# Kernel tuning notes

Hardware: AMD Instinct MI355X
Metric: run time of the kernel (lower is better)

The kernel has to match this reference:

```python
import jax, jax.numpy as jnp
import numpy as np

E = 16        # n_routed_experts
K = 2         # n_activated_experts (top-k)
DIM = 1024    # model dim
INTER = 704   # moe_inter_dim
B, S = 4, 1024


def setup_inputs() -> dict:
    key = jax.random.key(0)
    ks = jax.random.split(key, 5)
    x = jax.random.normal(ks[0], (B, S, DIM), dtype=jnp.float32)
    Wg = jax.random.normal(ks[1], (E, DIM), dtype=jnp.float32) * 0.02   # gate (Linear, no bias)
    W1 = jax.random.normal(ks[2], (E, DIM, INTER), dtype=jnp.float32) * 0.02
    W3 = jax.random.normal(ks[3], (E, DIM, INTER), dtype=jnp.float32) * 0.02
    W2 = jax.random.normal(ks[4], (E, INTER, DIM), dtype=jnp.float32) * 0.02
    return {"x": x, "Wg": Wg, "W1": W1, "W2": W2, "W3": W3}


def reference(x, Wg, W1, W2, W3):
    # Single-process semantics of MoEWithAll2All: the all2all dispatch/combine is
    # pure communication; the math is: softmax router -> top-k -> renormalize ->
    # per-expert SwiGLU MLP on routed tokens -> weighted combine at original slots.
    Bb, Ss, D = x.shape
    xf = x.reshape(-1, D)                              # [N, D], N = B*S
    logits = xf @ Wg.T                                 # [N, E]
    probs = jax.nn.softmax(logits, axis=-1)
    topw, topi = jax.lax.top_k(probs, K)               # [N, K]
    topw = topw / topw.sum(axis=-1, keepdims=True)
    # gates[n, e] = routed weight of token n for expert e (0 if not routed):
    # identical math to the masked gather/scatter dispatch in the original.
    gates = (jax.nn.one_hot(topi, E, dtype=xf.dtype) * topw[..., None]).sum(axis=1)  # [N, E]
    out = jnp.zeros_like(xf)
    for e in range(E):                                 # small fixed loop over experts
        h = jax.nn.silu(xf @ W1[e]) * (xf @ W3[e])     # SwiGLU expert, [N, INTER]
        out = out + gates[:, e:e + 1] * (h @ W2[e])    # combine with gate weights
    return out.reshape(Bb, Ss, D)
```

## Files before the change

kernel.cpp:

```cpp
#include <hip/hip_runtime.h>

#define NTOK 4096
#define DDIM 1024
#define IDIM 704
#define NEXP 16
#define NSLOT 8192
#define MAXT 128
#define NPAD1 768

typedef __attribute__((ext_vector_type(8))) short bf16x8;
typedef __attribute__((ext_vector_type(4))) float f32x4;
typedef __attribute__((ext_vector_type(4))) unsigned short us4;
typedef __attribute__((ext_vector_type(8))) unsigned short us8;

__device__ __forceinline__ unsigned short f2bf(float f) {
  union { float f; unsigned int u; } v; v.f = f;
  unsigned int r = v.u + 0x7fffu + ((v.u >> 16) & 1u);
  return (unsigned short)(r >> 16);
}

__device__ __forceinline__ void gload_lds16(const void* g, void* l) {
  __builtin_amdgcn_global_load_lds((const __attribute__((address_space(1))) void*)g,
                                   (__attribute__((address_space(3))) void*)l, 16, 0, 0);
}

__global__ void k_router(const float* __restrict__ x, const float* __restrict__ Wg,
                         int* __restrict__ tok_e, float* __restrict__ tok_w,
                         unsigned short* __restrict__ Xb) {
  int lane = threadIdx.x & 63;
  int wv = threadIdx.x >> 6;
  int t = blockIdx.x * 4 + wv;
  const f32x4* xr = (const f32x4*)(x + (size_t)t * DDIM);
  us4* xbr = (us4*)(Xb + (size_t)t * DDIM);
  f32x4 xv[4];
#pragma unroll
  for (int c = 0; c < 4; ++c) {
    xv[c] = xr[c * 64 + lane];
    us4 o;
#pragma unroll
    for (int j = 0; j < 4; ++j) o[j] = f2bf(xv[c][j]);
    xbr[c * 64 + lane] = o;
  }
  float p[NEXP];
#pragma unroll
  for (int e = 0; e < NEXP; ++e) {
    const f32x4* wr = (const f32x4*)(Wg + (size_t)e * DDIM);
    float s = 0.f;
#pragma unroll
    for (int c = 0; c < 4; ++c) {
      f32x4 w4 = wr[c * 64 + lane];
      s += xv[c][0]*w4[0] + xv[c][1]*w4[1] + xv[c][2]*w4[2] + xv[c][3]*w4[3];
    }
    p[e] = s;
  }
#pragma unroll
  for (int off = 32; off >= 1; off >>= 1) {
#pragma unroll
    for (int e = 0; e < NEXP; ++e) p[e] += __shfl_xor(p[e], off);
  }
  int i0 = 0; float b0 = p[0];
#pragma unroll
  for (int e = 1; e < NEXP; ++e) if (p[e] > b0) { b0 = p[e]; i0 = e; }
  int i1 = -1; float b1 = -3.4e38f;
#pragma unroll
  for (int e = 0; e < NEXP; ++e) if (e != i0 && p[e] > b1) { b1 = p[e]; i1 = e; }
  if (lane == 0) {
    float w0 = 1.f / (1.f + __expf(b1 - b0));
    tok_e[2*t] = i0; tok_e[2*t+1] = i1;
    tok_w[2*t] = w0; tok_w[2*t+1] = 1.f - w0;
  }
}

__global__ void k_scan_scatter(const int* __restrict__ tok_e, const float* __restrict__ tok_w,
                               int* __restrict__ counts, int* __restrict__ offsets,
                               int* __restrict__ ntiles, int* __restrict__ tile_e,
                               int* __restrict__ tile_m0, int* __restrict__ token_map,
                               float* __restrict__ gate_w, int* __restrict__ slot_of) {
  int eb = blockIdx.x;
  int t = threadIdx.x, lane = t & 63, wv = t >> 6;
  __shared__ int h[256 * 17];
  __shared__ int counts_s[NEXP];
  __shared__ int wsum[4];
  int te[32]; float tw[32];
#pragma unroll
  for (int c = 0; c < 32; ++c) {
    te[c] = tok_e[c * 256 + t];
    tw[c] = tok_w[c * 256 + t];
  }
  int c[NEXP];
#pragma unroll
  for (int e = 0; e < NEXP; ++e) c[e] = 0;
#pragma unroll
  for (int i = 0; i < 32; ++i) {
#pragma unroll
    for (int e = 0; e < NEXP; ++e) c[e] += (te[i] == e) ? 1 : 0;
  }
#pragma unroll
  for (int e = 0; e < NEXP; ++e) h[t * 17 + e] = c[e];
  __syncthreads();
  if (t < NEXP) {
    int s = 0;
    for (int i = 0; i < 256; ++i) s += h[i * 17 + t];
    counts_s[t] = s;
    if (eb == 0) counts[t] = s;
  }
  __syncthreads();
  int off_e = 0;
#pragma unroll
  for (int e = 0; e < NEXP; ++e) off_e += (e < eb) ? counts_s[e] : 0;
  if (eb == 0 && t == 0) {
    int acc = 0, nt = 0;
    for (int e = 0; e < NEXP; ++e) {
      offsets[e] = acc;
      int cc = counts_s[e];
      for (int m0 = 0; m0 < cc; m0 += 128) { tile_e[nt] = e; tile_m0[nt] = m0; ++nt; }
      acc += cc;
    }
    offsets[NEXP] = acc;
    *ntiles = nt;
  }
  int run = off_e;
  unsigned long long below = (lane == 63) ? 0x7fffffffffffffffull : ((1ull << lane) - 1ull);
#pragma unroll 1
  for (int cc = 0; cc < 32; ++cc) {
    bool f = (te[cc] == eb);
    unsigned long long m = __ballot(f);
    if (lane == 0) wsum[wv] = __popcll(m);
    __syncthreads();
    int base = run;
    for (int w = 0; w < wv; ++w) base += wsum[w];
    int tot = wsum[0] + wsum[1] + wsum[2] + wsum[3];
    if (f) {
      int i = cc * 256 + t;
      int slot = base + __popcll(m & below);
      token_map[slot] = i >> 1;
      gate_w[slot] = tw[cc];
      slot_of[i] = slot;
    }
    run += tot;
    __syncthreads();
  }
}

__global__ void k_wtrans_all(const float* __restrict__ W1, const float* __restrict__ W3,
                             const float* __restrict__ W2, unsigned short* __restrict__ W1T,
                             unsigned short* __restrict__ W3T, unsigned short* __restrict__ W2T) {
  int b = blockIdx.x;
  const float* src; unsigned short* dst;
  int ksz, nsz, kx, np, e;
  if (b < 3072) {
    int which = (b >= 1536) ? 1 : 0;
    int tb = b - which * 1536;
    kx = tb & 15; int rest = tb >> 4; np = rest % 6; e = rest / 6;
    ksz = DDIM; nsz = IDIM;
    src = (which ? W3 : W1) + (size_t)e * DDIM * IDIM;
    dst = (which ? W3T : W1T) + (size_t)e * NPAD1 * DDIM;
  } else {
    int tb = b - 3072;
    kx = tb % 11; int rest = tb / 11; np = rest & 7; e = rest >> 3;
    ksz = IDIM; nsz = DDIM;
    src = W2 + (size_t)e * IDIM * DDIM;
    dst = W2T + (size_t)e * DDIM * IDIM;
  }
  int k0 = kx * 64;
  __shared__ unsigned short lds[64 * 64];
  int t = threadIdx.x;
#pragma unroll
  for (int p = 0; p < 2; ++p) {
    int n0 = np * 128 + p * 64;
    if (p) __syncthreads();
    if (n0 >= nsz) {
      int nr = t >> 3, kc0 = (t & 7) * 8;
      us8 z = (us8)(unsigned short)0;
#pragma unroll
      for (int q = 0; q < 2; ++q)
        *(us8*)(dst + (size_t)(n0 + nr + q * 32) * ksz + k0 + kc0) = z;
      continue;
    }
    int kr4 = (t >> 4) * 4, nc4 = (t & 15) * 4;
    f32x4 v[4];
#pragma unroll
    for (int j = 0; j < 4; ++j)
      v[j] = *(const f32x4*)(src + (size_t)(k0 + kr4 + j) * nsz + n0 + nc4);
    int c8 = kr4 >> 3, half = (kr4 >> 2) & 1;
#pragma unroll
    for (int i = 0; i < 4; ++i) {
      us4 o;
#pragma unroll
      for (int j = 0; j < 4; ++j) o[j] = f2bf(v[j][i]);
      int row = nc4 + i;
      int addr = row * 64 + ((c8 ^ ((row >> 2) & 7)) << 3) + half * 4;
      *(us4*)(lds + addr) = o;
    }
    __syncthreads();
    int nr = t >> 3, kc8 = t & 7;
#pragma unroll
    for (int q = 0; q < 2; ++q) {
      int row = nr + q * 32;
      us8 o = *(const us8*)(lds + row * 64 + ((kc8 ^ ((row >> 2) & 7)) << 3));
      *(us8*)(dst + (size_t)(n0 + row) * ksz + k0 + kc8 * 8) = o;
    }
  }
}

__global__ __launch_bounds__(256, 2)
void k_gemm1(const unsigned short* __restrict__ Xb, const unsigned short* __restrict__ W1T,
             const unsigned short* __restrict__ W3T, const int* __restrict__ token_map,
             const float* __restrict__ gate_w, const int* __restrict__ ntiles,
             const int* __restrict__ tile_e, const int* __restrict__ tile_m0,
             const int* __restrict__ offsets, const int* __restrict__ counts,
             unsigned short* __restrict__ H) {
  int idx = blockIdx.x;
  int xcd = idx & 7, r = idx >> 3;
  int g = (r >> 2) * 8 + xcd;
  int mm = r & 3;
  int ty = (g / 6) * 4 + mm;
  if (ty >= *ntiles) return;
  int n0 = (g % 6) * 128;
  int e = tile_e[ty], m0 = tile_m0[ty];
  int base_slot = offsets[e] + m0;
  int cnt = counts[e] - m0; if (cnt > 128) cnt = 128;

  __shared__ unsigned short As[2][128 * 32];
  __shared__ unsigned short B1s[2][128 * 32];
  __shared__ unsigned short B3s[2][128 * 32];

  int t = threadIdx.x;
  int row = t >> 2, kc = (t & 3) * 8;
  int r0i = base_slot + row;      if (r0i > NSLOT - 1) r0i = NSLOT - 1;
  int r1i = base_slot + 64 + row; if (r1i > NSLOT - 1) r1i = NSLOT - 1;
  const unsigned short* ag0 = Xb + (size_t)token_map[r0i] * DDIM + kc;
  const unsigned short* ag1 = Xb + (size_t)token_map[r1i] * DDIM + kc;
  const unsigned short* b1g0 = W1T + ((size_t)e * NPAD1 + n0 + row) * DDIM + kc;
  const unsigned short* b1g1 = b1g0 + (size_t)64 * DDIM;
  const unsigned short* b3g0 = W3T + ((size_t)e * NPAD1 + n0 + row) * DDIM + kc;
  const unsigned short* b3g1 = b3g0 + (size_t)64 * DDIM;
  int d0 = t * 8, d1 = 2048 + t * 8;

  int lane = t & 63, wv = t >> 6;
  int wm = (wv >> 1) * 64, wn = (wv & 1) * 64;
  int lm = lane & 15, kg = lane >> 4;
  int ao[4], bo[4];
#pragma unroll
  for (int i = 0; i < 4; ++i) {
    ao[i] = (wm + i * 16 + lm) * 32 + kg * 8;
    bo[i] = (wn + i * 16 + lm) * 32 + kg * 8;
  }

  f32x4 acc1[4][4], acc3[4][4];
#pragma unroll
  for (int i = 0; i < 4; ++i)
#pragma unroll
    for (int j = 0; j < 4; ++j) { acc1[i][j] = 0.f; acc3[i][j] = 0.f; }

  gload_lds16(ag0, As[0] + d0);
  gload_lds16(ag1, As[0] + d1);
  gload_lds16(b1g0, B1s[0] + d0);
  gload_lds16(b1g1, B1s[0] + d1);
  gload_lds16(b3g0, B3s[0] + d0);
  gload_lds16(b3g1, B3s[0] + d1);

  for (int k0 = 0; k0 < DDIM; k0 += 32) {
    int cur = (k0 >> 5) & 1;
    __syncthreads();
    if (k0 + 32 < DDIM) {
      int nx = cur ^ 1, kn = k0 + 32;
      gload_lds16(ag0 + kn, As[nx] + d0);
      gload_lds16(ag1 + kn, As[nx] + d1);
      gload_lds16(b1g0 + kn, B1s[nx] + d0);
      gload_lds16(b1g1 + kn, B1s[nx] + d1);
      gload_lds16(b3g0 + kn, B3s[nx] + d0);
      gload_lds16(b3g1 + kn, B3s[nx] + d1);
    }
    bf16x8 av[4], b1v[4], b3v[4];
#pragma unroll
    for (int i = 0; i < 4; ++i) {
      av[i]  = *(const bf16x8*)(As[cur] + ao[i]);
      b1v[i] = *(const bf16x8*)(B1s[cur] + bo[i]);
      b3v[i] = *(const bf16x8*)(B3s[cur] + bo[i]);
    }
#pragma unroll
    for (int mi = 0; mi < 4; ++mi)
#pragma unroll
      for (int ni = 0; ni < 4; ++ni) {
        acc1[mi][ni] = __builtin_amdgcn_mfma_f32_16x16x32_bf16(av[mi], b1v[ni], acc1[mi][ni], 0, 0, 0);
        acc3[mi][ni] = __builtin_amdgcn_mfma_f32_16x16x32_bf16(av[mi], b3v[ni], acc3[mi][ni], 0, 0, 0);
      }
  }

#pragma unroll
  for (int mi = 0; mi < 4; ++mi)
#pragma unroll
    for (int rr = 0; rr < 4; ++rr) {
      int orow = wm + mi * 16 + kg * 4 + rr;
      if (orow < cnt) {
        int slot = base_slot + orow;
        float gw = gate_w[slot];
        unsigned short* hrow = H + (size_t)slot * IDIM;
#pragma unroll
        for (int ni = 0; ni < 4; ++ni) {
          int nn = n0 + wn + ni * 16 + lm;
          if (nn < IDIM) {
            float v1 = acc1[mi][ni][rr];
            float v3 = acc3[mi][ni][rr];
            float h = v1 / (1.f + __expf(-v1)) * v3 * gw;
            hrow[nn] = f2bf(h);
          }
        }
      }
    }
}

__global__ __launch_bounds__(256, 3)
void k_gemm2(const unsigned short* __restrict__ H, const unsigned short* __restrict__ W2T,
             const int* __restrict__ ntiles, const int* __restrict__ tile_e,
             const int* __restrict__ tile_m0, const int* __restrict__ offsets,
             const int* __restrict__ counts, float* __restrict__ O2) {
  int idx = blockIdx.x;
  int xcd = idx & 7, r = idx >> 3;
  int g = (r >> 2) * 8 + xcd;
  int mm = r & 3;
  int ty = (g >> 3) * 4 + mm;
  if (ty >= *ntiles) return;
  int n0 = (g & 7) * 128;
  int e = tile_e[ty], m0 = tile_m0[ty];
  int base_slot = offsets[e] + m0;
  int cnt = counts[e] - m0; if (cnt > 128) cnt = 128;

  __shared__ unsigned short As[2][128 * 32];
  __shared__ unsigned short Bs[2][128 * 32];

  int t = threadIdx.x;
  int row = t >> 2, kc = (t & 3) * 8;
  int r0i = base_slot + row;      if (r0i > NSLOT - 1) r0i = NSLOT - 1;
  int r1i = base_slot + 64 + row; if (r1i > NSLOT - 1) r1i = NSLOT - 1;
  const unsigned short* ag0 = H + (size_t)r0i * IDIM + kc;
  const unsigned short* ag1 = H + (size_t)r1i * IDIM + kc;
  const unsigned short* bg0 = W2T + ((size_t)e * DDIM + n0 + row) * IDIM + kc;
  const unsigned short* bg1 = bg0 + (size_t)64 * IDIM;
  int d0 = t * 8, d1 = 2048 + t * 8;

  int lane = t & 63, wv = t >> 6;
  int wm = (wv >> 1) * 64, wn = (wv & 1) * 64;
  int lm = lane & 15, kg = lane >> 4;
  int ao[4], bo[4];
#pragma unroll
  for (int i = 0; i < 4; ++i) {
    ao[i] = (wm + i * 16 + lm) * 32 + kg * 8;
    bo[i] = (wn + i * 16 + lm) * 32 + kg * 8;
  }

  f32x4 acc[4][4];
#pragma unroll
  for (int i = 0; i < 4; ++i)
#pragma unroll
    for (int j = 0; j < 4; ++j) acc[i][j] = 0.f;

  gload_lds16(ag0, As[0] + d0);
  gload_lds16(ag1, As[0] + d1);
  gload_lds16(bg0, Bs[0] + d0);
  gload_lds16(bg1, Bs[0] + d1);

  for (int k0 = 0; k0 < IDIM; k0 += 32) {
    int cur = (k0 >> 5) & 1;
    __syncthreads();
    if (k0 + 32 < IDIM) {
      int nx = cur ^ 1, kn = k0 + 32;
      gload_lds16(ag0 + kn, As[nx] + d0);
      gload_lds16(ag1 + kn, As[nx] + d1);
      gload_lds16(bg0 + kn, Bs[nx] + d0);
      gload_lds16(bg1 + kn, Bs[nx] + d1);
    }
    bf16x8 av[4], bv[4];
#pragma unroll
    for (int i = 0; i < 4; ++i) {
      av[i] = *(const bf16x8*)(As[cur] + ao[i]);
      bv[i] = *(const bf16x8*)(Bs[cur] + bo[i]);
    }
#pragma unroll
    for (int mi = 0; mi < 4; ++mi)
#pragma unroll
      for (int ni = 0; ni < 4; ++ni)
        acc[mi][ni] = __builtin_amdgcn_mfma_f32_16x16x32_bf16(av[mi], bv[ni], acc[mi][ni], 0, 0, 0);
  }

#pragma unroll
  for (int mi = 0; mi < 4; ++mi)
#pragma unroll
    for (int rr = 0; rr < 4; ++rr) {
      int orow = wm + mi * 16 + kg * 4 + rr;
      if (orow < cnt) {
        float* op = O2 + (size_t)(base_slot + orow) * DDIM + n0;
#pragma unroll
        for (int ni = 0; ni < 4; ++ni)
          op[wn + ni * 16 + lm] = acc[mi][ni][rr];
      }
    }
}

__global__ void k_combine(const float* __restrict__ O2, const int* __restrict__ slot_of,
                          float* __restrict__ out) {
  int tk = blockIdx.x, tt = threadIdx.x;
  int s0 = slot_of[2 * tk], s1 = slot_of[2 * tk + 1];
  f32x4 a = ((const f32x4*)(O2 + (size_t)s0 * DDIM))[tt];
  f32x4 b = ((const f32x4*)(O2 + (size_t)s1 * DDIM))[tt];
  ((f32x4*)(out + (size_t)tk * DDIM))[tt] = a + b;
}

extern "C" void kernel_launch(void* const* d_in, const int* in_sizes, int n_in,
                              void* d_out, int out_size, void* d_ws, size_t ws_size,
                              hipStream_t stream) {
  const float* x  = (const float*)d_in[0];
  const float* Wg = (const float*)d_in[1];
  const float* W1 = (const float*)d_in[2];
  const float* W2 = (const float*)d_in[3];
  const float* W3 = (const float*)d_in[4];
  float* out = (float*)d_out;

  char* ws = (char*)d_ws;
  size_t off = 0;
  unsigned short* Xb = (unsigned short*)(ws + off); off += (size_t)NTOK * DDIM * 2;
  unsigned short* H  = (unsigned short*)(ws + off); off += (size_t)NSLOT * IDIM * 2;
  float* O2 = (float*)(ws + off); off += (size_t)NSLOT * DDIM * 4;
  unsigned short* W1T = (unsigned short*)(ws + off); off += (size_t)NEXP * NPAD1 * DDIM * 2;
  unsigned short* W3T = (unsigned short*)(ws + off); off += (size_t)NEXP * NPAD1 * DDIM * 2;
  unsigned short* W2T = (unsigned short*)(ws + off); off += (size_t)NEXP * DDIM * IDIM * 2;
  int* counts  = (int*)(ws + off); off += 64;
  int* offsets = (int*)(ws + off); off += 128;
  int* ntiles  = (int*)(ws + off); off += 64;
  int* tile_e  = (int*)(ws + off); off += MAXT * 4;
  int* tile_m0 = (int*)(ws + off); off += MAXT * 4;
  int* tok_e   = (int*)(ws + off); off += NSLOT * 4;
  float* tok_w = (float*)(ws + off); off += NSLOT * 4;
  int* token_map = (int*)(ws + off); off += NSLOT * 4;
  float* gate_w  = (float*)(ws + off); off += NSLOT * 4;
  int* slot_of   = (int*)(ws + off); off += NSLOT * 4;

  k_router<<<1024, 256, 0, stream>>>(x, Wg, tok_e, tok_w, Xb);
  k_scan_scatter<<<NEXP, 256, 0, stream>>>(tok_e, tok_w, counts, offsets, ntiles,
                                           tile_e, tile_m0, token_map, gate_w, slot_of);
  k_wtrans_all<<<4480, 256, 0, stream>>>(W1, W3, W2, W1T, W3T, W2T);
  k_gemm1<<<480, 256, 0, stream>>>(Xb, W1T, W3T, token_map, gate_w, ntiles, tile_e,
                                   tile_m0, offsets, counts, H);
  k_gemm2<<<640, 256, 0, stream>>>(H, W2T, ntiles, tile_e, tile_m0, offsets, counts, O2);
  k_combine<<<4096, 256, 0, stream>>>(O2, slot_of, out);
}
```

Measured before the change: 312.1 us.

## Fuse router with weight transpose kernel and store expert outputs in bf16

Merges the router and the weight-conversion/transpose work into one kernel launch, where block index picks the role, and removes a separate launch. The transpose blocks now load both 64-column halves up front into two LDS buffers, so there is one barrier instead of a serialized two-pass loop. The per-slot expert outputs are stored as bf16 instead of fp32, halving the write traffic of gemm2 and the read traffic of combine. The cost is some extra rounding error in the combined output.

```diff
diff --git a/kernel.cpp b/kernel.cpp
--- a/kernel.cpp
+++ b/kernel.cpp
@@ -7,6 +7,7 @@
 #define NSLOT 8192
 #define MAXT 128
 #define NPAD1 768
+#define WTBLK 4480
 
 typedef __attribute__((ext_vector_type(8))) short bf16x8;
 typedef __attribute__((ext_vector_type(4))) float f32x4;
@@ -19,19 +20,90 @@
   return (unsigned short)(r >> 16);
 }
 
+__device__ __forceinline__ float bf2f(unsigned short b) {
+  union { unsigned int u; float f; } v; v.u = ((unsigned int)b) << 16;
+  return v.f;
+}
+
 __device__ __forceinline__ void gload_lds16(const void* g, void* l) {
   __builtin_amdgcn_global_load_lds((const __attribute__((address_space(1))) void*)g,
                                    (__attribute__((address_space(3))) void*)l, 16, 0, 0);
 }
 
-__global__ void k_router(const float* __restrict__ x, const float* __restrict__ Wg,
-                         int* __restrict__ tok_e, float* __restrict__ tok_w,
-                         unsigned short* __restrict__ Xb) {
+__global__ void k_front(const float* __restrict__ x, const float* __restrict__ Wg,
+                        const float* __restrict__ W1, const float* __restrict__ W3,
+                        const float* __restrict__ W2, int* __restrict__ tok_e,
+                        float* __restrict__ tok_w, unsigned short* __restrict__ Xb,
+                        unsigned short* __restrict__ W1T, unsigned short* __restrict__ W3T,
+                        unsigned short* __restrict__ W2T) {
+  int b = blockIdx.x;
+  if (b < WTBLK) {
+    __shared__ unsigned short lds[2][64 * 64];
+    const float* src; unsigned short* dst;
+    int ksz, nsz, kx, np, e;
+    if (b < 3072) {
+      int which = (b >= 1536) ? 1 : 0;
+      int tb = b - which * 1536;
+      kx = tb & 15; int rest = tb >> 4; np = rest % 6; e = rest / 6;
+      ksz = DDIM; nsz = IDIM;
+      src = (which ? W3 : W1) + (size_t)e * DDIM * IDIM;
+      dst = (which ? W3T : W1T) + (size_t)e * NPAD1 * DDIM;
+    } else {
+      int tb = b - 3072;
+      kx = tb % 11; int rest = tb / 11; np = rest & 7; e = rest >> 3;
+      ksz = IDIM; nsz = DDIM;
+      src = W2 + (size_t)e * IDIM * DDIM;
+      dst = W2T + (size_t)e * DDIM * IDIM;
+    }
+    int k0 = kx * 64;
+    int t = threadIdx.x;
+    int kr4 = (t >> 4) * 4, nc4 = (t & 15) * 4;
+    int n0a = np * 128, n0b = n0a + 64;
+    bool bvalid = n0b < nsz;
+    f32x4 v0[4], v1[4];
+#pragma unroll
+    for (int j = 0; j < 4; ++j)
+      v0[j] = *(const f32x4*)(src + (size_t)(k0 + kr4 + j) * nsz + n0a + nc4);
+    if (bvalid) {
+#pragma unroll
+      for (int j = 0; j < 4; ++j)
+        v1[j] = *(const f32x4*)(src + (size_t)(k0 + kr4 + j) * nsz + n0b + nc4);
+    }
+    int c8 = kr4 >> 3, half = (kr4 >> 2) & 1;
+#pragma unroll
+    for (int i = 0; i < 4; ++i) {
+      int row = nc4 + i;
+      int addr = row * 64 + ((c8 ^ ((row >> 2) & 7)) << 3) + half * 4;
+      us4 o0;
+#pragma unroll
+      for (int j = 0; j < 4; ++j) o0[j] = f2bf(v0[j][i]);
+      *(us4*)(lds[0] + addr) = o0;
+      if (bvalid) {
+        us4 o1;
+#pragma unroll
+        for (int j = 0; j < 4; ++j) o1[j] = f2bf(v1[j][i]);
+        *(us4*)(lds[1] + addr) = o1;
+      }
+    }
+    __syncthreads();
+    int nr = t >> 3, kc8 = t & 7;
+#pragma unroll
+    for (int q = 0; q < 2; ++q) {
+      int row = nr + q * 32;
+      us8 oA = *(const us8*)(lds[0] + row * 64 + ((kc8 ^ ((row >> 2) & 7)) << 3));
+      *(us8*)(dst + (size_t)(n0a + row) * ksz + k0 + kc8 * 8) = oA;
+      us8 oB = bvalid ? *(const us8*)(lds[1] + row * 64 + ((kc8 ^ ((row >> 2) & 7)) << 3))
+                      : (us8)(unsigned short)0;
+      *(us8*)(dst + (size_t)(n0b + row) * ksz + k0 + kc8 * 8) = oB;
+    }
+    return;
+  }
+  int rb = b - WTBLK;
   int lane = threadIdx.x & 63;
   int wv = threadIdx.x >> 6;
-  int t = blockIdx.x * 4 + wv;
-  const f32x4* xr = (const f32x4*)(x + (size_t)t * DDIM);
-  us4* xbr = (us4*)(Xb + (size_t)t * DDIM);
+  int tk = rb * 4 + wv;
+  const f32x4* xr = (const f32x4*)(x + (size_t)tk * DDIM);
+  us4* xbr = (us4*)(Xb + (size_t)tk * DDIM);
   f32x4 xv[4];
 #pragma unroll
   for (int c = 0; c < 4; ++c) {
@@ -66,8 +138,8 @@
   for (int e = 0; e < NEXP; ++e) if (e != i0 && p[e] > b1) { b1 = p[e]; i1 = e; }
   if (lane == 0) {
     float w0 = 1.f / (1.f + __expf(b1 - b0));
-    tok_e[2*t] = i0; tok_e[2*t+1] = i1;
-    tok_w[2*t] = w0; tok_w[2*t+1] = 1.f - w0;
+    tok_e[2*tk] = i0; tok_e[2*tk+1] = i1;
+    tok_w[2*tk] = w0; tok_w[2*tk+1] = 1.f - w0;
   }
 }
 
@@ -142,67 +214,6 @@
   }
 }
 
-__global__ void k_wtrans_all(const float* __restrict__ W1, const float* __restrict__ W3,
-                             const float* __restrict__ W2, unsigned short* __restrict__ W1T,
-                             unsigned short* __restrict__ W3T, unsigned short* __restrict__ W2T) {
-  int b = blockIdx.x;
-  const float* src; unsigned short* dst;
-  int ksz, nsz, kx, np, e;
-  if (b < 3072) {
-    int which = (b >= 1536) ? 1 : 0;
-    int tb = b - which * 1536;
-    kx = tb & 15; int rest = tb >> 4; np = rest % 6; e = rest / 6;
-    ksz = DDIM; nsz = IDIM;
-    src = (which ? W3 : W1) + (size_t)e * DDIM * IDIM;
-    dst = (which ? W3T : W1T) + (size_t)e * NPAD1 * DDIM;
-  } else {
-    int tb = b - 3072;
-    kx = tb % 11; int rest = tb / 11; np = rest & 7; e = rest >> 3;
-    ksz = IDIM; nsz = DDIM;
-    src = W2 + (size_t)e * IDIM * DDIM;
-    dst = W2T + (size_t)e * DDIM * IDIM;
-  }
-  int k0 = kx * 64;
-  __shared__ unsigned short lds[64 * 64];
-  int t = threadIdx.x;
-#pragma unroll
-  for (int p = 0; p < 2; ++p) {
-    int n0 = np * 128 + p * 64;
-    if (p) __syncthreads();
-    if (n0 >= nsz) {
-      int nr = t >> 3, kc0 = (t & 7) * 8;
-      us8 z = (us8)(unsigned short)0;
-#pragma unroll
-      for (int q = 0; q < 2; ++q)
-        *(us8*)(dst + (size_t)(n0 + nr + q * 32) * ksz + k0 + kc0) = z;
-      continue;
-    }
-    int kr4 = (t >> 4) * 4, nc4 = (t & 15) * 4;
-    f32x4 v[4];
-#pragma unroll
-    for (int j = 0; j < 4; ++j)
-      v[j] = *(const f32x4*)(src + (size_t)(k0 + kr4 + j) * nsz + n0 + nc4);
-    int c8 = kr4 >> 3, half = (kr4 >> 2) & 1;
-#pragma unroll
-    for (int i = 0; i < 4; ++i) {
-      us4 o;
-#pragma unroll
-      for (int j = 0; j < 4; ++j) o[j] = f2bf(v[j][i]);
-      int row = nc4 + i;
-      int addr = row * 64 + ((c8 ^ ((row >> 2) & 7)) << 3) + half * 4;
-      *(us4*)(lds + addr) = o;
-    }
-    __syncthreads();
-    int nr = t >> 3, kc8 = t & 7;
-#pragma unroll
-    for (int q = 0; q < 2; ++q) {
-      int row = nr + q * 32;
-      us8 o = *(const us8*)(lds + row * 64 + ((kc8 ^ ((row >> 2) & 7)) << 3));
-      *(us8*)(dst + (size_t)(n0 + row) * ksz + k0 + kc8 * 8) = o;
-    }
-  }
-}
-
 __global__ __launch_bounds__(256, 2)
 void k_gemm1(const unsigned short* __restrict__ Xb, const unsigned short* __restrict__ W1T,
              const unsigned short* __restrict__ W3T, const int* __restrict__ token_map,
@@ -303,8 +314,8 @@
           if (nn < IDIM) {
             float v1 = acc1[mi][ni][rr];
             float v3 = acc3[mi][ni][rr];
-            float h = v1 / (1.f + __expf(-v1)) * v3 * gw;
-            hrow[nn] = f2bf(h);
+            float hh = v1 / (1.f + __expf(-v1)) * v3 * gw;
+            hrow[nn] = f2bf(hh);
           }
         }
       }
@@ -315,7 +326,7 @@
 void k_gemm2(const unsigned short* __restrict__ H, const unsigned short* __restrict__ W2T,
              const int* __restrict__ ntiles, const int* __restrict__ tile_e,
              const int* __restrict__ tile_m0, const int* __restrict__ offsets,
-             const int* __restrict__ counts, float* __restrict__ O2) {
+             const int* __restrict__ counts, unsigned short* __restrict__ O2) {
   int idx = blockIdx.x;
   int xcd = idx & 7, r = idx >> 3;
   int g = (r >> 2) * 8 + xcd;
@@ -390,21 +401,24 @@
     for (int rr = 0; rr < 4; ++rr) {
       int orow = wm + mi * 16 + kg * 4 + rr;
       if (orow < cnt) {
-        float* op = O2 + (size_t)(base_slot + orow) * DDIM + n0;
+        unsigned short* op = O2 + (size_t)(base_slot + orow) * DDIM + n0;
 #pragma unroll
         for (int ni = 0; ni < 4; ++ni)
-          op[wn + ni * 16 + lm] = acc[mi][ni][rr];
+          op[wn + ni * 16 + lm] = f2bf(acc[mi][ni][rr]);
       }
     }
 }
 
-__global__ void k_combine(const float* __restrict__ O2, const int* __restrict__ slot_of,
+__global__ void k_combine(const unsigned short* __restrict__ O2, const int* __restrict__ slot_of,
                           float* __restrict__ out) {
   int tk = blockIdx.x, tt = threadIdx.x;
   int s0 = slot_of[2 * tk], s1 = slot_of[2 * tk + 1];
-  f32x4 a = ((const f32x4*)(O2 + (size_t)s0 * DDIM))[tt];
-  f32x4 b = ((const f32x4*)(O2 + (size_t)s1 * DDIM))[tt];
-  ((f32x4*)(out + (size_t)tk * DDIM))[tt] = a + b;
+  us4 a = ((const us4*)(O2 + (size_t)s0 * DDIM))[tt];
+  us4 b = ((const us4*)(O2 + (size_t)s1 * DDIM))[tt];
+  f32x4 o;
+#pragma unroll
+  for (int j = 0; j < 4; ++j) o[j] = bf2f(a[j]) + bf2f(b[j]);
+  ((f32x4*)(out + (size_t)tk * DDIM))[tt] = o;
 }
 
 extern "C" void kernel_launch(void* const* d_in, const int* in_sizes, int n_in,
@@ -421,7 +435,7 @@
   size_t off = 0;
   unsigned short* Xb = (unsigned short*)(ws + off); off += (size_t)NTOK * DDIM * 2;
   unsigned short* H  = (unsigned short*)(ws + off); off += (size_t)NSLOT * IDIM * 2;
-  float* O2 = (float*)(ws + off); off += (size_t)NSLOT * DDIM * 4;
+  unsigned short* O2 = (unsigned short*)(ws + off); off += (size_t)NSLOT * DDIM * 2;
   unsigned short* W1T = (unsigned short*)(ws + off); off += (size_t)NEXP * NPAD1 * DDIM * 2;
   unsigned short* W3T = (unsigned short*)(ws + off); off += (size_t)NEXP * NPAD1 * DDIM * 2;
   unsigned short* W2T = (unsigned short*)(ws + off); off += (size_t)NEXP * DDIM * IDIM * 2;
@@ -436,10 +450,10 @@
   float* gate_w  = (float*)(ws + off); off += NSLOT * 4;
   int* slot_of   = (int*)(ws + off); off += NSLOT * 4;
 
-  k_router<<<1024, 256, 0, stream>>>(x, Wg, tok_e, tok_w, Xb);
+  k_front<<<WTBLK + 1024, 256, 0, stream>>>(x, Wg, W1, W3, W2, tok_e, tok_w, Xb,
+                                            W1T, W3T, W2T);
   k_scan_scatter<<<NEXP, 256, 0, stream>>>(tok_e, tok_w, counts, offsets, ntiles,
                                            tile_e, tile_m0, token_map, gate_w, slot_of);
-  k_wtrans_all<<<4480, 256, 0, stream>>>(W1, W3, W2, W1T, W3T, W2T);
   k_gemm1<<<480, 256, 0, stream>>>(Xb, W1T, W3T, token_map, gate_w, ntiles, tile_e,
                                    tile_m0, offsets, counts, H);
   k_gemm2<<<640, 256, 0, stream>>>(H, W2T, ntiles, tile_e, tile_m0, offsets, counts, O2);
```

New measurement: 301.9 us. -3.3%, faster.
